# Optimization experiments

Measured on AMD Instinct MI355X. Metric: run time of the kernel, lower is better.

## Reference

```python
import jax, jax.numpy as jnp
import numpy as np

B, T, D = 4, 2048, 1024
H = 16
HD = D // H
NORM = float(np.sqrt(D))  # module uses sqrt(out_features), not sqrt(head_dim)


def setup_inputs() -> dict:
    key = jax.random.key(0)
    k1, k2, k3 = jax.random.split(key, 3)
    x = jax.random.normal(k1, (B, T, D), dtype=jnp.float32)
    w_qkv = jax.random.normal(k2, (D, 3 * D), dtype=jnp.float32) * (1.0 / np.sqrt(D))
    w_proj = jax.random.normal(k3, (D, D), dtype=jnp.float32) * (1.0 / np.sqrt(D))
    return {"x": x, "w_qkv": w_qkv, "w_proj": w_proj}


def reference(x, w_qkv, w_proj):
    b, t, _ = x.shape
    qkv = jnp.einsum('btd,de->bte', x, w_qkv)  # [B,T,3D]
    q, k, v = jnp.split(qkv, 3, axis=-1)
    # [B,H,T,HD]
    q = q.reshape(b, t, H, HD).transpose(0, 2, 1, 3)
    k = k.reshape(b, t, H, HD).transpose(0, 2, 1, 3)
    v = v.reshape(b, t, H, HD).transpose(0, 2, 1, 3)
    attn = jnp.einsum('bhqd,bhkd->bhqk', q, k) / NORM
    causal = jnp.tril(jnp.ones((t, t), dtype=bool))
    attn = jnp.where(causal[None, None], attn, -jnp.inf)
    attn = jax.nn.softmax(attn, axis=-1)
    y = jnp.einsum('bhqk,bhkd->bhqd', attn, v)
    out = y.transpose(0, 2, 1, 3).reshape(b, t, D)
    return jnp.einsum('btd,de->bte', out, w_proj)
```

## Files before the change

### kernel.cpp

```cpp
#include <hip/hip_runtime.h>
#include <hip/hip_bf16.h>
#include <cstdint>
#include <cstddef>

typedef __bf16 bfx8 __attribute__((ext_vector_type(8)));
typedef float  fx4  __attribute__((ext_vector_type(4)));
typedef float  fx16 __attribute__((ext_vector_type(16)));

#define MFMA_B16(a, b, c)  __builtin_amdgcn_mfma_f32_16x16x32_bf16((a), (b), (c), 0, 0, 0)
#define MFMA32(a, b, c)    __builtin_amdgcn_mfma_f32_32x32x16_bf16((a), (b), (c), 0, 0, 0)

#define GLD_LDS16(gsrc, ldst)                                                  \
  __builtin_amdgcn_global_load_lds(                                            \
      (const __attribute__((address_space(1))) void*)(gsrc),                   \
      (__attribute__((address_space(3))) void*)(ldst), 16, 0, 0)

static __device__ __forceinline__ unsigned short f2bf(float f) {
  union { float f; unsigned u; } v; v.f = f;
  unsigned r = v.u + 0x7fffu + ((v.u >> 16) & 1u);
  return (unsigned short)(r >> 16);
}

static __device__ __forceinline__ bfx8 ldb8(const void* p) {
  return *(const bfx8*)p;
}

static __device__ __forceinline__ unsigned pk2(float lo, float hi) {
  __hip_bfloat162 h2 = __float22bfloat162_rn(make_float2(lo, hi));
  union { __hip_bfloat162 h; unsigned u; } c; c.h = h2; return c.u;
}

static __device__ __forceinline__ bfx8 scale8(bfx8 x, float s) {
  union { bfx8 v; unsigned u[4]; } a; a.v = x;
  union { bfx8 v; unsigned u[4]; } r;
#pragma unroll
  for (int j = 0; j < 4; ++j) {
    union { unsigned u; float f; } lo, hi;
    lo.u = a.u[j] << 16;
    hi.u = a.u[j] & 0xffff0000u;
    r.u[j] = pk2(lo.f * s, hi.f * s);
  }
  return r.v;
}

#define BB 4
#define TT 2048
#define DD 1024
#define HH 16
#define HD 64

__global__ void k_cast(const float* __restrict__ in, unsigned short* __restrict__ out, int n) {
  int i = (blockIdx.x * blockDim.x + threadIdx.x) * 4;
  int stride = gridDim.x * blockDim.x * 4;
  for (; i < n; i += stride) {
    float4 v = *(const float4*)(in + i);
    ushort4 o;
    o.x = f2bf(v.x); o.y = f2bf(v.y); o.z = f2bf(v.z); o.w = f2bf(v.w);
    *(ushort4*)(out + i) = o;
  }
}

__global__ void k_transpose(const float* __restrict__ in, unsigned short* __restrict__ out,
                            int R, int C) {
  __shared__ float tile[32][33];
  int c0 = blockIdx.x * 32, r0 = blockIdx.y * 32;
  int tx = threadIdx.x, ty = threadIdx.y;
#pragma unroll
  for (int dy = 0; dy < 32; dy += 8)
    tile[ty + dy][tx] = in[(size_t)(r0 + ty + dy) * C + (c0 + tx)];
  __syncthreads();
#pragma unroll
  for (int dy = 0; dy < 32; dy += 8)
    out[(size_t)(c0 + ty + dy) * R + (r0 + tx)] = f2bf(tile[tx][ty + dy]);
}

template <int EPI>
__global__ __launch_bounds__(256) void k_gemm(
    const unsigned short* __restrict__ A,
    const unsigned short* __restrict__ Bt,
    float* __restrict__ outf,
    int M, int N, int K,
    unsigned short* __restrict__ qb, unsigned short* __restrict__ kb,
    unsigned short* __restrict__ vtb) {
  constexpr int BM = 128, BN = 128, BK = 32;
  __shared__ __align__(16) unsigned short As[BM * BK];
  __shared__ __align__(16) unsigned short Bs[BN * BK];

  const int tid  = threadIdx.x;
  const int lane = tid & 63;
  const int w    = tid >> 6;
  const int wr   = w >> 1, wc = w & 1;
  const int n16  = lane & 15, g = lane >> 4;
  const int m0 = blockIdx.y * BM, n0 = blockIdx.x * BN;

  fx4 acc[4][4] = {};

  for (int k0 = 0; k0 < K; k0 += BK) {
#pragma unroll
    for (int iss = 0; iss < 2; ++iss) {
      int bo   = iss * 4096 + w * 1024 + lane * 16;
      int row  = bo >> 6;
      int colb = bo & 63;
      const char* srcA = (const char*)A  + ((size_t)(m0 + row) * K + k0) * 2 + colb;
      const char* srcB = (const char*)Bt + ((size_t)(n0 + row) * K + k0) * 2 + colb;
      GLD_LDS16(srcA, (char*)As + iss * 4096 + w * 1024);
      GLD_LDS16(srcB, (char*)Bs + iss * 4096 + w * 1024);
    }
    __syncthreads();

    bfx8 af[4], bf[4];
#pragma unroll
    for (int mi = 0; mi < 4; ++mi)
      af[mi] = *(const bfx8*)(const void*)&As[(wr * 64 + mi * 16 + n16) * BK + g * 8];
#pragma unroll
    for (int ni = 0; ni < 4; ++ni)
      bf[ni] = *(const bfx8*)(const void*)&Bs[(wc * 64 + ni * 16 + n16) * BK + g * 8];
#pragma unroll
    for (int mi = 0; mi < 4; ++mi)
#pragma unroll
      for (int ni = 0; ni < 4; ++ni)
        acc[mi][ni] = MFMA_B16(af[mi], bf[ni], acc[mi][ni]);
    __syncthreads();
  }

#pragma unroll
  for (int mi = 0; mi < 4; ++mi) {
#pragma unroll
    for (int ni = 0; ni < 4; ++ni) {
      int mrow = m0 + wr * 64 + mi * 16 + g * 4;
      int ncol = n0 + wc * 64 + ni * 16 + n16;
      if (EPI == 0) {
#pragma unroll
        for (int i = 0; i < 4; ++i)
          outf[(size_t)(mrow + i) * N + ncol] = acc[mi][ni][i];
      } else {
        int sec = ncol >> 10;
        int h   = (ncol >> 6) & 15;
        int d   = ncol & 63;
#pragma unroll
        for (int i = 0; i < 4; ++i) {
          int mm = mrow + i;
          int b  = mm >> 11;
          int t  = mm & 2047;
          unsigned short val = f2bf(acc[mi][ni][i]);
          if (sec == 0)
            qb[(((size_t)(b * HH + h) * TT + t) << 6) + d] = val;
          else if (sec == 1)
            kb[(((size_t)(b * HH + h) * TT + t) << 6) + d] = val;
          else
            vtb[((size_t)(b * HH + h) * HD + d) * TT + t] = val;
        }
      }
    }
  }
}


static __device__ __forceinline__ void stage64(
    const char* __restrict__ kbb, const char* __restrict__ vbb, size_t kv0,
    char* ldsK, char* ldsV, int w, int lane) {
  int dest = w * 1024 + lane * 16;
  int row  = dest >> 7;
  int colb = dest & 127;
  int scol = colb ^ ((row & 7) << 4);
  GLD_LDS16(kbb + (kv0 + row) * 128 + scol, ldsK + w * 1024);
  GLD_LDS16(vbb + (size_t)row * (TT * 2) + kv0 * 2 + scol, ldsV + w * 1024);
}

static __device__ __forceinline__ void attn_tile_lds(
    const char* __restrict__ kbuf, const char* __restrict__ vbuf, int tt,
    const bfx8* qf, int lim, int hi, int l31,
    float& m, float& l, fx16& o0, fx16& o1) {
  const int r7 = (l31 & 7) << 4;
  const char* krow = kbuf + (size_t)(tt * 32 + l31) * 128;
  bfx8 kf0 = ldb8(krow + ((hi * 16 +  0) ^ r7));
  bfx8 kf1 = ldb8(krow + ((hi * 16 + 32) ^ r7));
  bfx8 kf2 = ldb8(krow + ((hi * 16 + 64) ^ r7));
  bfx8 kf3 = ldb8(krow + ((hi * 16 + 96) ^ r7));
  const char* vrow0 = vbuf + (size_t)l31 * 128;
  const char* vrow1 = vbuf + (size_t)(l31 + 32) * 128;
  const int c0 = (tt * 64 + hi * 16) ^ r7;
  const int c1 = (tt * 64 + 32 + hi * 16) ^ r7;
  bfx8 vf0 = ldb8(vrow0 + c0), vf1 = ldb8(vrow0 + c1);
  bfx8 vf2 = ldb8(vrow1 + c0), vf3 = ldb8(vrow1 + c1);

  fx16 s = {};
  s = MFMA32(kf0, qf[0], s);
  s = MFMA32(kf1, qf[1], s);
  s = MFMA32(kf2, qf[2], s);
  s = MFMA32(kf3, qf[3], s);

  float t[16];
#pragma unroll
  for (int r = 0; r < 16; ++r) {
    int koff = (r & 3) + 8 * (r >> 2);
    t[r] = (koff <= lim) ? s[r] : -__builtin_inff();
  }
  float x0 = fmaxf(t[0], t[1]),   x1 = fmaxf(t[2], t[3]);
  float x2 = fmaxf(t[4], t[5]),   x3 = fmaxf(t[6], t[7]);
  float x4 = fmaxf(t[8], t[9]),   x5 = fmaxf(t[10], t[11]);
  float x6 = fmaxf(t[12], t[13]), x7 = fmaxf(t[14], t[15]);
  float y0 = fmaxf(x0, x1), y1 = fmaxf(x2, x3), y2 = fmaxf(x4, x5), y3 = fmaxf(x6, x7);
  float mx = fmaxf(fmaxf(y0, y1), fmaxf(y2, y3));

  bool need = mx > m + 8.0f;
  if (__ballot(need) != 0ull) {
    float mo   = fmaxf(mx, __shfl_xor(mx, 32));
    float mnew = fmaxf(m, mo);
    float alpha = __builtin_amdgcn_exp2f(m - mnew);
    m = mnew;
    l *= alpha;
#pragma unroll
    for (int r = 0; r < 16; ++r) { o0[r] *= alpha; o1[r] *= alpha; }
  }

  float p[16];
#pragma unroll
  for (int r = 0; r < 16; ++r) p[r] = __builtin_amdgcn_exp2f(t[r] - m);
  float s0 = (p[0] + p[1]) + (p[2] + p[3]);
  float s1 = (p[4] + p[5]) + (p[6] + p[7]);
  float s2 = (p[8] + p[9]) + (p[10] + p[11]);
  float s3 = (p[12] + p[13]) + (p[14] + p[15]);
  l += (s0 + s1) + (s2 + s3);

  union { unsigned u[4]; bfx8 v; } P0, P1;
#pragma unroll
  for (int c = 0; c < 2; ++c) {
    unsigned a0 = pk2(p[8*c+0], p[8*c+1]);
    unsigned a1 = pk2(p[8*c+2], p[8*c+3]);
    unsigned b0 = pk2(p[8*c+4], p[8*c+5]);
    unsigned b1 = pk2(p[8*c+6], p[8*c+7]);
    unsigned xa0 = __shfl_xor(a0, 32), xa1 = __shfl_xor(a1, 32);
    unsigned xb0 = __shfl_xor(b0, 32), xb1 = __shfl_xor(b1, 32);
    unsigned* U = c ? P1.u : P0.u;
    U[0] = hi ? xb0 : a0;
    U[1] = hi ? xb1 : a1;
    U[2] = hi ? b0 : xa0;
    U[3] = hi ? b1 : xa1;
  }
  o0 = MFMA32(vf0, P0.v, o0);
  o0 = MFMA32(vf1, P1.v, o0);
  o1 = MFMA32(vf2, P0.v, o1);
  o1 = MFMA32(vf3, P1.v, o1);
}

__global__ __launch_bounds__(512) void k_attn(
    const unsigned short* __restrict__ qb,
    const unsigned short* __restrict__ kb,
    const unsigned short* __restrict__ vtb,
    unsigned short* __restrict__ yb) {
  __shared__ __align__(16) unsigned short Ks[2][4096];
  __shared__ __align__(16) unsigned short Vs[2][4096];

  const int tid  = threadIdx.x;
  const int lane = tid & 63;
  const int w    = tid >> 6;
  const int l31  = lane & 31;
  const int hi   = lane >> 5;

  int blk = blockIdx.x;
  const int s = 7 - (blk & 7);
  const int h = (blk >> 3) & 15;
  const int b = blk >> 7;
  const size_t bh = (size_t)b * HH + h;

  const int qw = s * 256 + w * 32;
  const int NC = 4 * (s + 1);

  const char* kbb = (const char*)(kb + bh * TT * HD);
  const char* vbb = (const char*)(vtb + bh * HD * TT);

  const float CL = 0.0450842346f;
  const unsigned short* qp = qb + (bh * TT + qw + l31) * HD + hi * 8;
  bfx8 qf[4];
#pragma unroll
  for (int dc = 0; dc < 4; ++dc) qf[dc] = scale8(ldb8(qp + dc * 16), CL);

  fx16 o0 = {}, o1 = {};
  float m = -__builtin_inff(), l = 0.f;
  const int limd = l31 - 4 * hi;
  const int BIG  = 127;

  stage64(kbb, vbb, 0, (char*)Ks[0], (char*)Vs[0], w, lane);
  __syncthreads();

  int cur = 0;
#pragma unroll 1
  for (int c = 0; c < NC; ++c) {
    if (c + 1 < NC)
      stage64(kbb, vbb, (size_t)(c + 1) * 64,
              (char*)Ks[cur ^ 1], (char*)Vs[cur ^ 1], w, lane);
    const char* kbuf = (const char*)Ks[cur];
    const char* vbuf = (const char*)Vs[cur];
    const int kv0 = c * 64;
    if (kv0 <= qw)
      attn_tile_lds(kbuf, vbuf, 0, qf, (kv0 == qw) ? limd : BIG, hi, l31, m, l, o0, o1);
    if (kv0 + 32 <= qw)
      attn_tile_lds(kbuf, vbuf, 1, qf, (kv0 + 32 == qw) ? limd : BIG, hi, l31, m, l, o0, o1);
    __syncthreads();
    cur ^= 1;
  }

  l += __shfl_xor(l, 32);
  float inv = 1.0f / l;
  unsigned short* yp = yb + (size_t)(b * TT + qw + l31) * DD + h * HD + 4 * hi;
#pragma unroll
  for (int g = 0; g < 4; ++g) {
    ushort4 s4;
    s4.x = f2bf(o0[4*g+0] * inv); s4.y = f2bf(o0[4*g+1] * inv);
    s4.z = f2bf(o0[4*g+2] * inv); s4.w = f2bf(o0[4*g+3] * inv);
    *(ushort4*)(yp + 8 * g) = s4;
    s4.x = f2bf(o1[4*g+0] * inv); s4.y = f2bf(o1[4*g+1] * inv);
    s4.z = f2bf(o1[4*g+2] * inv); s4.w = f2bf(o1[4*g+3] * inv);
    *(ushort4*)(yp + 32 + 8 * g) = s4;
  }
}

extern "C" void kernel_launch(void* const* d_in, const int* in_sizes, int n_in,
                              void* d_out, int out_size, void* d_ws, size_t ws_size,
                              hipStream_t stream) {
  const float* x      = (const float*)d_in[0];
  const float* w_qkv  = (const float*)d_in[1];
  const float* w_proj = (const float*)d_in[2];
  float* out = (float*)d_out;

  char* ws = (char*)d_ws;
  unsigned short* xb     = (unsigned short*)(ws);
  unsigned short* wqkvT  = (unsigned short*)(ws + (size_t)(16u << 20));
  unsigned short* wprojT = (unsigned short*)(ws + (size_t)(22u << 20));
  unsigned short* qb     = (unsigned short*)(ws + (size_t)(24u << 20));
  unsigned short* kb     = (unsigned short*)(ws + (size_t)(40u << 20));
  unsigned short* vtb    = (unsigned short*)(ws + (size_t)(56u << 20));
  unsigned short* yb     = xb;

  k_cast<<<4096, 256, 0, stream>>>(x, xb, BB * TT * DD);

  dim3 tb(32, 8);
  k_transpose<<<dim3(3 * DD / 32, DD / 32), tb, 0, stream>>>(w_qkv, wqkvT, DD, 3 * DD);
  k_transpose<<<dim3(DD / 32, DD / 32), tb, 0, stream>>>(w_proj, wprojT, DD, DD);

  k_gemm<1><<<dim3(3 * DD / 128, BB * TT / 128), 256, 0, stream>>>(
      xb, wqkvT, nullptr, BB * TT, 3 * DD, DD, qb, kb, vtb);

  k_attn<<<BB * HH * 8, 512, 0, stream>>>(qb, kb, vtb, yb);

  k_gemm<0><<<dim3(DD / 128, BB * TT / 128), 256, 0, stream>>>(
      yb, wprojT, out, BB * TT, DD, DD, nullptr, nullptr, nullptr);
}
```

Baseline: 291.4 us.

## Pre-permute V layout, halve attention block size, and use finer-grained pipeline waits

```diff
diff --git a/kernel.cpp b/kernel.cpp
--- a/kernel.cpp
+++ b/kernel.cpp
@@ -21,8 +21,11 @@
   return (unsigned short)(r >> 16);
 }
 
-static __device__ __forceinline__ bfx8 ldb8(const void* p) {
-  return *(const bfx8*)p;
+static __device__ __forceinline__ bfx8 ldb8(const unsigned short* p) {
+  return *(const bfx8*)(const void*)p;
+}
+static __device__ __forceinline__ bfx8 ldb8c(const char* p) {
+  return *(const bfx8*)(const void*)p;
 }
 
 static __device__ __forceinline__ unsigned pk2(float lo, float hi) {
@@ -147,8 +150,13 @@
             qb[(((size_t)(b * HH + h) * TT + t) << 6) + d] = val;
           else if (sec == 1)
             kb[(((size_t)(b * HH + h) * TT + t) << 6) + d] = val;
-          else
-            vtb[((size_t)(b * HH + h) * HD + d) * TT + t] = val;
+          else {
+            int hik = (t >> 2) & 1;
+            int fq  = (t >> 4) & 1;
+            int o   = (t & 3) + (((t >> 3) & 1) << 2);
+            int tp  = (t & ~31) | (((fq << 1) | hik) << 3) | o;
+            vtb[((size_t)(b * HH + h) * HD + d) * TT + tp] = val;
+          }
         }
       }
     }
@@ -157,32 +165,38 @@
 
 
 static __device__ __forceinline__ void stage64(
-    const char* __restrict__ kbb, const char* __restrict__ vbb, size_t kv0,
-    char* ldsK, char* ldsV, int w, int lane) {
-  int dest = w * 1024 + lane * 16;
-  int row  = dest >> 7;
-  int colb = dest & 127;
-  int scol = colb ^ ((row & 7) << 4);
-  GLD_LDS16(kbb + (kv0 + row) * 128 + scol, ldsK + w * 1024);
-  GLD_LDS16(vbb + (size_t)row * (TT * 2) + kv0 * 2 + scol, ldsV + w * 1024);
+    const char* __restrict__ kbb, const char* __restrict__ vbb, int kv0,
+    char* __restrict__ buf, int w, int lane) {
+  const int L    = w * 64 + lane;
+  const int r    = L >> 3;
+  const int sl   = L & 7;
+  const int slog = sl ^ (r & 7);
+#pragma unroll
+  for (int u = 0; u < 2; ++u) {
+    int row = u * 32 + r;
+    GLD_LDS16(kbb + (size_t)(kv0 + row) * 128 + slog * 16,
+              buf + u * 4096 + w * 1024);
+    GLD_LDS16(vbb + (size_t)row * (TT * 2) + (size_t)kv0 * 2 + slog * 16,
+              buf + 8192 + u * 4096 + w * 1024);
+  }
 }
 
 static __device__ __forceinline__ void attn_tile_lds(
-    const char* __restrict__ kbuf, const char* __restrict__ vbuf, int tt,
+    const char* __restrict__ kb_, const char* __restrict__ vb_, int tt,
     const bfx8* qf, int lim, int hi, int l31,
     float& m, float& l, fx16& o0, fx16& o1) {
-  const int r7 = (l31 & 7) << 4;
-  const char* krow = kbuf + (size_t)(tt * 32 + l31) * 128;
-  bfx8 kf0 = ldb8(krow + ((hi * 16 +  0) ^ r7));
-  bfx8 kf1 = ldb8(krow + ((hi * 16 + 32) ^ r7));
-  bfx8 kf2 = ldb8(krow + ((hi * 16 + 64) ^ r7));
-  bfx8 kf3 = ldb8(krow + ((hi * 16 + 96) ^ r7));
-  const char* vrow0 = vbuf + (size_t)l31 * 128;
-  const char* vrow1 = vbuf + (size_t)(l31 + 32) * 128;
-  const int c0 = (tt * 64 + hi * 16) ^ r7;
-  const int c1 = (tt * 64 + 32 + hi * 16) ^ r7;
-  bfx8 vf0 = ldb8(vrow0 + c0), vf1 = ldb8(vrow0 + c1);
-  bfx8 vf2 = ldb8(vrow1 + c0), vf3 = ldb8(vrow1 + c1);
+  const int sw = (l31 & 7) << 4;
+  const char* kr = kb_ + (size_t)(tt * 32 + l31) * 128;
+  bfx8 kf0 = ldb8c(kr + (((0 + hi) << 4) ^ sw));
+  bfx8 kf1 = ldb8c(kr + (((2 + hi) << 4) ^ sw));
+  bfx8 kf2 = ldb8c(kr + (((4 + hi) << 4) ^ sw));
+  bfx8 kf3 = ldb8c(kr + (((6 + hi) << 4) ^ sw));
+  const char* vr  = vb_ + (size_t)l31 * 128;
+  const char* vr2 = vb_ + (size_t)(l31 + 32) * 128;
+  const int s0v = ((tt * 4 + 0 + hi) << 4) ^ sw;
+  const int s1v = ((tt * 4 + 2 + hi) << 4) ^ sw;
+  bfx8 vf0 = ldb8c(vr + s0v),  vf1 = ldb8c(vr + s1v);
+  bfx8 vf2 = ldb8c(vr2 + s0v), vf3 = ldb8c(vr2 + s1v);
 
   fx16 s = {};
   s = MFMA32(kf0, qf[0], s);
@@ -224,33 +238,23 @@
   l += (s0 + s1) + (s2 + s3);
 
   union { unsigned u[4]; bfx8 v; } P0, P1;
-#pragma unroll
-  for (int c = 0; c < 2; ++c) {
-    unsigned a0 = pk2(p[8*c+0], p[8*c+1]);
-    unsigned a1 = pk2(p[8*c+2], p[8*c+3]);
-    unsigned b0 = pk2(p[8*c+4], p[8*c+5]);
-    unsigned b1 = pk2(p[8*c+6], p[8*c+7]);
-    unsigned xa0 = __shfl_xor(a0, 32), xa1 = __shfl_xor(a1, 32);
-    unsigned xb0 = __shfl_xor(b0, 32), xb1 = __shfl_xor(b1, 32);
-    unsigned* U = c ? P1.u : P0.u;
-    U[0] = hi ? xb0 : a0;
-    U[1] = hi ? xb1 : a1;
-    U[2] = hi ? b0 : xa0;
-    U[3] = hi ? b1 : xa1;
-  }
+  P0.u[0] = pk2(p[0],  p[1]);   P0.u[1] = pk2(p[2],  p[3]);
+  P0.u[2] = pk2(p[4],  p[5]);   P0.u[3] = pk2(p[6],  p[7]);
+  P1.u[0] = pk2(p[8],  p[9]);   P1.u[1] = pk2(p[10], p[11]);
+  P1.u[2] = pk2(p[12], p[13]);  P1.u[3] = pk2(p[14], p[15]);
+
   o0 = MFMA32(vf0, P0.v, o0);
   o0 = MFMA32(vf1, P1.v, o0);
   o1 = MFMA32(vf2, P0.v, o1);
   o1 = MFMA32(vf3, P1.v, o1);
 }
 
-__global__ __launch_bounds__(512) void k_attn(
+__global__ __launch_bounds__(256) void k_attn(
     const unsigned short* __restrict__ qb,
     const unsigned short* __restrict__ kb,
     const unsigned short* __restrict__ vtb,
     unsigned short* __restrict__ yb) {
-  __shared__ __align__(16) unsigned short Ks[2][4096];
-  __shared__ __align__(16) unsigned short Vs[2][4096];
+  __shared__ __align__(16) char Ls[2][16384];
 
   const int tid  = threadIdx.x;
   const int lane = tid & 63;
@@ -258,20 +262,19 @@
   const int l31  = lane & 31;
   const int hi   = lane >> 5;
 
-  int blk = blockIdx.x;
-  const int s = 7 - (blk & 7);
-  const int h = (blk >> 3) & 15;
-  const int b = blk >> 7;
-  const size_t bh = (size_t)b * HH + h;
-
-  const int qw = s * 256 + w * 32;
-  const int NC = 4 * (s + 1);
-
-  const char* kbb = (const char*)(kb + bh * TT * HD);
-  const char* vbb = (const char*)(vtb + bh * HD * TT);
+  const int blk = blockIdx.x;
+  const int q16 = blk & 15;
+  const int bh  = blk >> 4;
+  const int cb  = (q16 < 8) ? (15 - q16) : (q16 - 8);
+  const int i   = cb * 4 + w;
+  const int NC  = 2 * cb + 2;
+  const int b   = bh >> 4, h = bh & 15;
+
+  const char* kbb = (const char*)(kb + (size_t)bh * TT * HD);
+  const char* vbb = (const char*)(vtb + (size_t)bh * HD * TT);
 
   const float CL = 0.0450842346f;
-  const unsigned short* qp = qb + (bh * TT + qw + l31) * HD + hi * 8;
+  const unsigned short* qp = qb + ((size_t)bh * TT + i * 32 + l31) * HD + hi * 8;
   bfx8 qf[4];
 #pragma unroll
   for (int dc = 0; dc < 4; ++dc) qf[dc] = scale8(ldb8(qp + dc * 16), CL);
@@ -279,31 +282,32 @@
   fx16 o0 = {}, o1 = {};
   float m = -__builtin_inff(), l = 0.f;
   const int limd = l31 - 4 * hi;
-  const int BIG  = 127;
-
-  stage64(kbb, vbb, 0, (char*)Ks[0], (char*)Vs[0], w, lane);
-  __syncthreads();
-
-  int cur = 0;
+
+  stage64(kbb, vbb, 0, Ls[0], w, lane);
+
 #pragma unroll 1
   for (int c = 0; c < NC; ++c) {
-    if (c + 1 < NC)
-      stage64(kbb, vbb, (size_t)(c + 1) * 64,
-              (char*)Ks[cur ^ 1], (char*)Vs[cur ^ 1], w, lane);
-    const char* kbuf = (const char*)Ks[cur];
-    const char* vbuf = (const char*)Vs[cur];
-    const int kv0 = c * 64;
-    if (kv0 <= qw)
-      attn_tile_lds(kbuf, vbuf, 0, qf, (kv0 == qw) ? limd : BIG, hi, l31, m, l, o0, o1);
-    if (kv0 + 32 <= qw)
-      attn_tile_lds(kbuf, vbuf, 1, qf, (kv0 + 32 == qw) ? limd : BIG, hi, l31, m, l, o0, o1);
-    __syncthreads();
-    cur ^= 1;
+    if (c + 1 < NC) {
+      stage64(kbb, vbb, (c + 1) * 64, Ls[(c + 1) & 1], w, lane);
+      asm volatile("s_waitcnt vmcnt(4)" ::: "memory");
+    } else {
+      asm volatile("s_waitcnt vmcnt(0)" ::: "memory");
+    }
+    asm volatile("s_barrier" ::: "memory");
+
+    const char* kbuf = Ls[c & 1];
+    const char* vbuf = Ls[c & 1] + 8192;
+    const int t0 = 2 * c, t1 = 2 * c + 1;
+    if (t0 <= i)
+      attn_tile_lds(kbuf, vbuf, 0, qf, (t0 == i) ? limd : 127, hi, l31, m, l, o0, o1);
+    if (t1 <= i)
+      attn_tile_lds(kbuf, vbuf, 1, qf, (t1 == i) ? limd : 127, hi, l31, m, l, o0, o1);
+    asm volatile("s_barrier" ::: "memory");
   }
 
   l += __shfl_xor(l, 32);
   float inv = 1.0f / l;
-  unsigned short* yp = yb + (size_t)(b * TT + qw + l31) * DD + h * HD + 4 * hi;
+  unsigned short* yp = yb + ((size_t)b * TT + i * 32 + l31) * DD + h * HD + 4 * hi;
 #pragma unroll
   for (int g = 0; g < 4; ++g) {
     ushort4 s4;
@@ -342,7 +346,7 @@
   k_gemm<1><<<dim3(3 * DD / 128, BB * TT / 128), 256, 0, stream>>>(
       xb, wqkvT, nullptr, BB * TT, 3 * DD, DD, qb, kb, vtb);
 
-  k_attn<<<BB * HH * 8, 512, 0, stream>>>(qb, kb, vtb, yb);
+  k_attn<<<64 * 16, 256, 0, stream>>>(qb, kb, vtb, yb);
 
   k_gemm<0><<<dim3(DD / 128, BB * TT / 128), 256, 0, stream>>>(
       yb, wprojT, out, BB * TT, DD, DD, nullptr, nullptr, nullptr);
```

After: 263.2 us. 9.7% less time.
